# Kernel optimization log

Hardware: AMD Instinct MI355X
Metric: run time of the kernel (lower is better)

The kernel has to match this reference:

```python
import jax, jax.numpy as jnp
import numpy as np

CHEB_K = 2  # hops per support; stacked terms = 1 + 2*CHEB_K = 5


def setup_inputs() -> dict:
    key = jax.random.key(0)
    k1, k2, k3, k4, k5 = jax.random.split(key, 5)
    B, N, C, O, D = 16, 1024, 64, 64, 10
    return {
        "x": jax.random.normal(k1, (B, N, C), dtype=jnp.float32),
        "adj": jax.random.uniform(k2, (2, B, N, N), dtype=jnp.float32),
        "node_embedding": jax.random.normal(k3, (N, D), dtype=jnp.float32),
        "weights_pool": jax.random.normal(k4, (D, 2 * CHEB_K + 1, C, O), dtype=jnp.float32) * 0.1,
        "bias_pool": jax.random.normal(k5, (D, O), dtype=jnp.float32) * 0.1,
    }


def reference(x, adj, node_embedding, weights_pool, bias_pool):
    # k-hop graph aggregation over each of the 2 supports
    out = [x]
    for s in range(adj.shape[0]):
        a = adj[s]  # [B, N, N]
        x1 = x
        for _ in range(CHEB_K):
            x1 = jnp.einsum('bnm,bmc->bnc', a, x1)
            out.append(x1)
    x_g = jnp.stack(out, axis=2)  # [B, N, K, C] with K = 2*cheb_k+1 (already node-major)
    # per-node hypernetwork weights and bias from node embeddings
    weights = jnp.einsum('nd,dkio->nkio', node_embedding, weights_pool)  # [N, K, C, O]
    bias = node_embedding @ bias_pool  # [N, O]
    # per-node contraction over (K, C)
    return jnp.einsum('bnki,nkio->bno', x_g, weights) + bias
```

## Files before the change

### kernel.cpp

```cpp
#include <hip/hip_runtime.h>
#include <stdint.h>


typedef __attribute__((ext_vector_type(4))) float f32x4;
typedef __attribute__((ext_vector_type(2))) float f32x2;
typedef __attribute__((ext_vector_type(8))) short s16x8;
typedef __attribute__((ext_vector_type(8))) __bf16 bf16x8;

__device__ __forceinline__ unsigned short f2bf(float f) {
  union { float f; uint32_t u; } v; v.f = f;
  uint32_t r = v.u + 0x7FFFu + ((v.u >> 16) & 1u);
  return (unsigned short)(r >> 16);
}
__device__ __forceinline__ uint32_t pack2(float a, float b) {
  return (uint32_t)f2bf(a) | ((uint32_t)f2bf(b) << 16);
}

union FragU { s16x8 s; bf16x8 b; uint32_t u[4]; };

__device__ __forceinline__ void async_cp16(const void* g, void* l) {
  __builtin_amdgcn_global_load_lds(
      (const __attribute__((address_space(1))) void*)g,
      (__attribute__((address_space(3))) void*)l, 16, 0, 0);
}

__global__ __launch_bounds__(256) void prep(const float* __restrict__ x,
                                            const float* __restrict__ wp,
                                            unsigned short* __restrict__ XT0,
                                            unsigned short* __restrict__ wpTb) {
  __shared__ __align__(16) char smem[17160];
  const int tid = threadIdx.x;
  const int bid = blockIdx.x;
  if (bid < 256) {
    unsigned short (*tl)[72] = (unsigned short(*)[72])smem;
    const int b = bid >> 4, n0 = (bid & 15) * 64;
    {
      const int c4 = (tid & 15) * 4;
#pragma unroll
      for (int i = 0; i < 4; ++i) {
        const int row = (tid >> 4) + i * 16;
        f32x4 v =
            *(const f32x4*)(x + ((size_t)(b * 1024 + n0 + row)) * 64 + c4);
        *(uint32_t*)&tl[row][c4]     = pack2(v[0], v[1]);
        *(uint32_t*)&tl[row][c4 + 2] = pack2(v[2], v[3]);
      }
    }
    __syncthreads();
    {
      const int c = tid >> 2;
      const int nch = (tid & 3) * 16;
      s16x8 s0, s1;
#pragma unroll
      for (int j = 0; j < 8; ++j) {
        s0[j] = (short)tl[nch + j][c];
        s1[j] = (short)tl[nch + 8 + j][c];
      }
      unsigned short* p = XT0 + (size_t)(b * 64 + c) * 1024 + n0 + nch;
      *(s16x8*)p = s0;
      *(s16x8*)(p + 8) = s1;
    }
  } else {
    float (*tl)[65] = (float(*)[65])smem;
    const int jj = bid - 256;
    const int d = jj / 5, ki0 = (jj % 5) * 64;
    const float* src = wp + (size_t)d * 20480;
    {
      const int o4 = (tid & 15) * 4;
#pragma unroll
      for (int i = 0; i < 4; ++i) {
        const int row = (tid >> 4) + i * 16;
        f32x4 v = *(const f32x4*)(src + (size_t)(ki0 + row) * 64 + o4);
        tl[row][o4] = v[0]; tl[row][o4 + 1] = v[1];
        tl[row][o4 + 2] = v[2]; tl[row][o4 + 3] = v[3];
      }
    }
    __syncthreads();
    {
      const int o = tid >> 2;
      const int kch = (tid & 3) * 16;
      unsigned short* dst =
          wpTb + (size_t)d * 20480 + (size_t)o * 320 + ki0 + kch;
      s16x8 s0, s1;
#pragma unroll
      for (int j = 0; j < 8; ++j) {
        s0[j] = (short)f2bf(tl[kch + j][o]);
        s1[j] = (short)f2bf(tl[kch + 8 + j][o]);
      }
      *(s16x8*)dst = s0;
      *(s16x8*)(dst + 8) = s1;
    }
  }
}

__device__ __forceinline__ void hop_body(
    char* smem, const float* __restrict__ A,
    const unsigned short* __restrict__ XT, unsigned short* __restrict__ Xoutb,
    unsigned short* __restrict__ XTout, int write_xt, int rowbase) {
  const int tid = threadIdx.x;
  const int wave = tid >> 6, lane = tid & 63;
  const int l15 = lane & 15, q = lane >> 4;

  float* const Ast = (float*)smem;
  unsigned short* const Bst = (unsigned short*)(smem + 32768);

  const float* asrc[4];
  int aldso[4];
#pragma unroll
  for (int i = 0; i < 4; ++i) {
    const int r = wave * 16 + i * 4 + (lane >> 4);
    const int gch = (lane & 15) ^ (r & 7);
    asrc[i] = A + (size_t)(rowbase + r) * 1024 + gch * 4;
    aldso[i] = (wave * 16 + i * 4) * 64;
  }
  const unsigned short* bsrc[2];
  int bldso[2];
#pragma unroll
  for (int i = 0; i < 2; ++i) {
    const int r = wave * 16 + i * 8 + (lane >> 3);
    bsrc[i] = XT + (size_t)r * 1024 + ((lane & 7) ^ (r & 7)) * 8;
    bldso[i] = (wave * 16 + i * 8) * 64;
  }

  f32x4 acc[4];
#pragma unroll
  for (int t = 0; t < 4; ++t) acc[t] = (f32x4){0.f, 0.f, 0.f, 0.f};

  auto issue = [&](int s, int k0) {
#pragma unroll
    for (int i = 0; i < 4; ++i)
      async_cp16(asrc[i] + k0, Ast + s * 4096 + aldso[i]);
#pragma unroll
    for (int i = 0; i < 2; ++i)
      async_cp16(bsrc[i] + k0, Bst + s * 4096 + bldso[i]);
  };
  const int sw = l15 & 7;
  auto compute = [&](int s) {
    const float* Ab = Ast + s * 4096 + (wave * 16 + l15) * 64;
    const unsigned short* Bb = Bst + s * 4096 + l15 * 64;
#pragma unroll
    for (int h = 0; h < 2; ++h) {
      const int g0 = h * 8 + q * 2;
      f32x4 lo = *(const f32x4*)(Ab + (g0 ^ sw) * 4);
      f32x4 hi = *(const f32x4*)(Ab + ((g0 + 1) ^ sw) * 4);
      FragU af;
      af.u[0] = pack2(lo[0], lo[1]);
      af.u[1] = pack2(lo[2], lo[3]);
      af.u[2] = pack2(hi[0], hi[1]);
      af.u[3] = pack2(hi[2], hi[3]);
      const int cko = ((h * 4 + q) ^ sw) * 8;
#pragma unroll
      for (int t = 0; t < 4; ++t) {
        FragU bf;
        bf.s = *(const s16x8*)(Bb + t * 1024 + cko);
        acc[t] = __builtin_amdgcn_mfma_f32_16x16x32_bf16(af.b, bf.b, acc[t],
                                                         0, 0, 0);
      }
    }
  };

  issue(0, 0);
#pragma unroll 1
  for (int kt = 0; kt < 16; ++kt) {
    const int cur = kt & 1;
    __syncthreads();
    if (kt + 1 < 16) issue(cur ^ 1, (kt + 1) * 64);
    compute(cur);
  }

  __syncthreads();
  float (*tile)[65] = (float(*)[65])smem;
#pragma unroll
  for (int t = 0; t < 4; ++t)
#pragma unroll
    for (int rr = 0; rr < 4; ++rr)
      tile[wave * 16 + q * 4 + rr][t * 16 + l15] = acc[t][rr];
  __syncthreads();

  {
    const int row = tid >> 2;
    const int cb = (tid & 3) * 16;
    unsigned short* __restrict__ outp =
        Xoutb + (size_t)(rowbase + row) * 64 + cb;
    s16x8 s0, s1;
#pragma unroll
    for (int j = 0; j < 8; ++j) {
      s0[j] = (short)f2bf(tile[row][cb + j]);
      s1[j] = (short)f2bf(tile[row][cb + 8 + j]);
    }
    *(s16x8*)outp = s0;
    *(s16x8*)(outp + 8) = s1;
  }
  if (write_xt) {
    const int c = tid >> 2;
    const int nch = (tid & 3) * 16;
    unsigned short* __restrict__ xtp = XTout + (size_t)c * 1024 + rowbase + nch;
    s16x8 s0, s1;
#pragma unroll
    for (int j = 0; j < 8; ++j) {
      s0[j] = (short)f2bf(tile[nch + j][c]);
      s1[j] = (short)f2bf(tile[nch + 8 + j][c]);
    }
    *(s16x8*)xtp = s0;
    *(s16x8*)(xtp + 8) = s1;
  }
}

__global__ __launch_bounds__(256, 3) void hop1_kernel(
    const float* __restrict__ adj, const unsigned short* __restrict__ XT0,
    unsigned short* __restrict__ X1b, unsigned short* __restrict__ XT1) {
  __shared__ __align__(16) char smem[49152];
  const int bx = blockIdx.x, slice = blockIdx.y, b = slice & 15;
  hop_body(smem, adj + (size_t)slice * 1048576, XT0 + (size_t)b * 65536,
           X1b + (size_t)slice * 65536, XT1 + (size_t)slice * 65536, 1,
           bx * 64);
}

__global__ __launch_bounds__(256, 3) void hop2_kernel(
    const float* __restrict__ adj, const unsigned short* __restrict__ XT1,
    unsigned short* __restrict__ X2b) {
  __shared__ __align__(16) char smem[49152];
  const int bx = 15 - (int)blockIdx.x;
  const int slice = 31 - (int)blockIdx.y;
  hop_body(smem, adj + (size_t)slice * 1048576, XT1 + (size_t)slice * 65536,
           X2b + (size_t)slice * 65536, (unsigned short*)0, 0, bx * 64);
}

__global__ __launch_bounds__(256, 2) void final_kernel(
    const float* __restrict__ x, const unsigned short* __restrict__ X1b,
    const unsigned short* __restrict__ X2b,
    const unsigned short* __restrict__ wpTb, const float* __restrict__ emb,
    const float* __restrict__ bias_pool, float* __restrict__ out) {
  __shared__ unsigned short xg[2][16][328];
  const int tid = threadIdx.x;
  const int node_base = blockIdx.x * 2;

  for (int u = tid; u < 5120; u += 256) {
    const int nd = u / 2560;
    int rem = u - nd * 2560;
    const int bb = rem / 160;
    const int kiu = rem - bb * 160;
    const int ki = kiu * 2;
    const int k = ki >> 6;
    const int c = ki & 63;
    const int nn = node_base + nd;
    uint32_t w;
    if (k == 0) {
      f32x2 v = *(const f32x2*)(x + ((size_t)bb * 1024 + nn) * 64 + c);
      w = pack2(v[0], v[1]);
    } else {
      const unsigned short* arr = (k == 1 || k == 3) ? X1b : X2b;
      const int s = (k >= 3) ? 1 : 0;
      w = *(const uint32_t*)(arr + ((size_t)(s * 16 + bb) * 1024 + nn) * 64 + c);
    }
    *(uint32_t*)&xg[nd][bb][ki] = w;
  }
  __syncthreads();

  const int wave = tid >> 6, lane = tid & 63;
  const int nd = wave >> 1, oh = wave & 1;
  const int l15 = lane & 15, q = lane >> 4;
  const int n = node_base + nd;

  FragU af[10];
#pragma unroll
  for (int ks = 0; ks < 10; ++ks)
    af[ks].s = *(const s16x8*)&xg[nd][l15][ks * 32 + q * 8];

  f32x4 acc[2];
  acc[0] = (f32x4){0.f, 0.f, 0.f, 0.f};
  acc[1] = (f32x4){0.f, 0.f, 0.f, 0.f};

  const unsigned short* wb0 = wpTb + (size_t)(oh * 32 + l15) * 320 + q * 8;
#pragma unroll 1
  for (int d = 0; d < 10; ++d) {
    const unsigned short* wd = wb0 + (size_t)d * 20480;
    f32x4 tmp[2];
    tmp[0] = (f32x4){0.f, 0.f, 0.f, 0.f};
    tmp[1] = (f32x4){0.f, 0.f, 0.f, 0.f};
#pragma unroll
    for (int ks = 0; ks < 10; ++ks) {
#pragma unroll
      for (int tt = 0; tt < 2; ++tt) {
        FragU bf;
        bf.s = *(const s16x8*)(wd + tt * 5120 + ks * 32);
        tmp[tt] = __builtin_amdgcn_mfma_f32_16x16x32_bf16(af[ks].b, bf.b,
                                                          tmp[tt], 0, 0, 0);
      }
    }
    const float e = emb[n * 10 + d];
#pragma unroll
    for (int tt = 0; tt < 2; ++tt)
#pragma unroll
      for (int rr = 0; rr < 4; ++rr)
        acc[tt][rr] += e * tmp[tt][rr];
  }

#pragma unroll
  for (int tt = 0; tt < 2; ++tt) {
    const int o = (oh * 2 + tt) * 16 + l15;
    float bv = 0.f;
#pragma unroll
    for (int d = 0; d < 10; ++d)
      bv += emb[n * 10 + d] * bias_pool[d * 64 + o];
#pragma unroll
    for (int rr = 0; rr < 4; ++rr) {
      const int bb = q * 4 + rr;
      out[((size_t)bb * 1024 + n) * 64 + o] = acc[tt][rr] + bv;
    }
  }
}

extern "C" void kernel_launch(void* const* d_in, const int* in_sizes, int n_in,
                              void* d_out, int out_size, void* d_ws,
                              size_t ws_size, hipStream_t stream) {
  const float* x   = (const float*)d_in[0];
  const float* adj = (const float*)d_in[1];
  const float* emb = (const float*)d_in[2];
  const float* wp  = (const float*)d_in[3];
  const float* bp  = (const float*)d_in[4];
  float* out = (float*)d_out;

  char* ws = (char*)d_ws;
  unsigned short* XT0  = (unsigned short*)(ws);
  unsigned short* XT1  = (unsigned short*)(ws + ((size_t)2 << 20));
  unsigned short* X1b  = (unsigned short*)(ws + ((size_t)6 << 20));
  unsigned short* X2b  = (unsigned short*)(ws + ((size_t)10 << 20));
  unsigned short* wpTb = (unsigned short*)(ws + ((size_t)14 << 20));

  prep<<<dim3(306), dim3(256), 0, stream>>>(x, wp, XT0, wpTb);
  hop1_kernel<<<dim3(16, 32), dim3(256), 0, stream>>>(adj, XT0, X1b, XT1);
  hop2_kernel<<<dim3(16, 32), dim3(256), 0, stream>>>(adj, XT1, X2b);
  final_kernel<<<dim3(512), dim3(256), 0, stream>>>(x, X1b, X2b, wpTb, emb,
                                                    bp, out);
}
```

Baseline: 290.9 us.

## Fuse all stages into one cooperative persistent kernel with register-resident adjacency

Replaces the four launches (prep, hop1, hop2, final) with a single cooperative kernel of 256 blocks that synchronise through a software grid barrier. Each block loads its 128-row slab of the fp32 adjacency once, converts it to bf16 and keeps it in 32 register fragments, then reuses it for both hops. This halves adjacency reads from HBM, which dominate traffic. It also adds a triple-buffered pipeline for the transposed feature tiles, an X0 bf16 copy, and a swizzled weight layout staged through LDS in the final stage. In exchange it costs heavy register pressure at 512 threads, spin-barrier overhead, and a dependence on all blocks being co-resident.

```diff
diff --git a/kernel.cpp b/kernel.cpp
--- a/kernel.cpp
+++ b/kernel.cpp
@@ -3,7 +3,6 @@
 
 
 typedef __attribute__((ext_vector_type(4))) float f32x4;
-typedef __attribute__((ext_vector_type(2))) float f32x2;
 typedef __attribute__((ext_vector_type(8))) short s16x8;
 typedef __attribute__((ext_vector_type(8))) __bf16 bf16x8;
 
@@ -24,147 +23,75 @@
       (__attribute__((address_space(3))) void*)l, 16, 0, 0);
 }
 
-__global__ __launch_bounds__(256) void prep(const float* __restrict__ x,
-                                            const float* __restrict__ wp,
-                                            unsigned short* __restrict__ XT0,
-                                            unsigned short* __restrict__ wpTb) {
-  __shared__ __align__(16) char smem[17160];
-  const int tid = threadIdx.x;
-  const int bid = blockIdx.x;
-  if (bid < 256) {
-    unsigned short (*tl)[72] = (unsigned short(*)[72])smem;
-    const int b = bid >> 4, n0 = (bid & 15) * 64;
-    {
-      const int c4 = (tid & 15) * 4;
-#pragma unroll
-      for (int i = 0; i < 4; ++i) {
-        const int row = (tid >> 4) + i * 16;
-        f32x4 v =
-            *(const f32x4*)(x + ((size_t)(b * 1024 + n0 + row)) * 64 + c4);
-        *(uint32_t*)&tl[row][c4]     = pack2(v[0], v[1]);
-        *(uint32_t*)&tl[row][c4 + 2] = pack2(v[2], v[3]);
-      }
-    }
-    __syncthreads();
-    {
-      const int c = tid >> 2;
-      const int nch = (tid & 3) * 16;
-      s16x8 s0, s1;
-#pragma unroll
-      for (int j = 0; j < 8; ++j) {
-        s0[j] = (short)tl[nch + j][c];
-        s1[j] = (short)tl[nch + 8 + j][c];
-      }
-      unsigned short* p = XT0 + (size_t)(b * 64 + c) * 1024 + n0 + nch;
-      *(s16x8*)p = s0;
-      *(s16x8*)(p + 8) = s1;
-    }
-  } else {
-    float (*tl)[65] = (float(*)[65])smem;
-    const int jj = bid - 256;
-    const int d = jj / 5, ki0 = (jj % 5) * 64;
-    const float* src = wp + (size_t)d * 20480;
-    {
-      const int o4 = (tid & 15) * 4;
-#pragma unroll
-      for (int i = 0; i < 4; ++i) {
-        const int row = (tid >> 4) + i * 16;
-        f32x4 v = *(const f32x4*)(src + (size_t)(ki0 + row) * 64 + o4);
-        tl[row][o4] = v[0]; tl[row][o4 + 1] = v[1];
-        tl[row][o4 + 2] = v[2]; tl[row][o4 + 3] = v[3];
-      }
-    }
-    __syncthreads();
-    {
-      const int o = tid >> 2;
-      const int kch = (tid & 3) * 16;
-      unsigned short* dst =
-          wpTb + (size_t)d * 20480 + (size_t)o * 320 + ki0 + kch;
-      s16x8 s0, s1;
-#pragma unroll
-      for (int j = 0; j < 8; ++j) {
-        s0[j] = (short)f2bf(tl[kch + j][o]);
-        s1[j] = (short)f2bf(tl[kch + 8 + j][o]);
-      }
-      *(s16x8*)dst = s0;
-      *(s16x8*)(dst + 8) = s1;
-    }
-  }
-}
-
-__device__ __forceinline__ void hop_body(
-    char* smem, const float* __restrict__ A,
-    const unsigned short* __restrict__ XT, unsigned short* __restrict__ Xoutb,
-    unsigned short* __restrict__ XTout, int write_xt, int rowbase) {
+__global__ __launch_bounds__(64) void init_bar(unsigned* bar) {
+  if (threadIdx.x < 2) bar[threadIdx.x] = 0u;
+}
+
+__device__ __forceinline__ void gbar(unsigned* bar) {
+  __syncthreads();
+  if (threadIdx.x == 0) {
+    __threadfence();
+    unsigned g = __hip_atomic_load(bar + 1, __ATOMIC_RELAXED,
+                                   __HIP_MEMORY_SCOPE_AGENT);
+    unsigned a = __hip_atomic_fetch_add(bar, 1u, __ATOMIC_ACQ_REL,
+                                        __HIP_MEMORY_SCOPE_AGENT);
+    if (a == 255u) {
+      __hip_atomic_store(bar, 0u, __ATOMIC_RELAXED, __HIP_MEMORY_SCOPE_AGENT);
+      __hip_atomic_store(bar + 1, g + 1u, __ATOMIC_RELEASE,
+                         __HIP_MEMORY_SCOPE_AGENT);
+    } else {
+      while (__hip_atomic_load(bar + 1, __ATOMIC_RELAXED,
+                               __HIP_MEMORY_SCOPE_AGENT) == g)
+        __builtin_amdgcn_s_sleep(2);
+    }
+    __threadfence();
+  }
+  __syncthreads();
+}
+
+__device__ __forceinline__ void hop128(char* smem, const FragU (&af)[32],
+                                       const unsigned short* __restrict__ XT,
+                                       unsigned short* __restrict__ Xoutb,
+                                       unsigned short* __restrict__ XTout,
+                                       const int write_xt) {
   const int tid = threadIdx.x;
   const int wave = tid >> 6, lane = tid & 63;
-  const int l15 = lane & 15, q = lane >> 4;
-
-  float* const Ast = (float*)smem;
-  unsigned short* const Bst = (unsigned short*)(smem + 32768);
-
-  const float* asrc[4];
-  int aldso[4];
-#pragma unroll
-  for (int i = 0; i < 4; ++i) {
-    const int r = wave * 16 + i * 4 + (lane >> 4);
-    const int gch = (lane & 15) ^ (r & 7);
-    asrc[i] = A + (size_t)(rowbase + r) * 1024 + gch * 4;
-    aldso[i] = (wave * 16 + i * 4) * 64;
-  }
-  const unsigned short* bsrc[2];
-  int bldso[2];
-#pragma unroll
-  for (int i = 0; i < 2; ++i) {
-    const int r = wave * 16 + i * 8 + (lane >> 3);
-    bsrc[i] = XT + (size_t)r * 1024 + ((lane & 7) ^ (r & 7)) * 8;
-    bldso[i] = (wave * 16 + i * 8) * 64;
-  }
+  const int l15 = lane & 15, q = lane >> 4, sw = l15 & 7;
+
+  unsigned short* const Bst = (unsigned short*)smem;
+  const int c = wave * 8 + (lane >> 3);
+  const unsigned short* bsrc =
+      XT + (size_t)c * 1024 + ((lane & 7) ^ (c & 7)) * 8;
+  unsigned short* const bdst = Bst + wave * 512;
 
   f32x4 acc[4];
 #pragma unroll
   for (int t = 0; t < 4; ++t) acc[t] = (f32x4){0.f, 0.f, 0.f, 0.f};
 
-  auto issue = [&](int s, int k0) {
-#pragma unroll
-    for (int i = 0; i < 4; ++i)
-      async_cp16(asrc[i] + k0, Ast + s * 4096 + aldso[i]);
-#pragma unroll
-    for (int i = 0; i < 2; ++i)
-      async_cp16(bsrc[i] + k0, Bst + s * 4096 + bldso[i]);
-  };
-  const int sw = l15 & 7;
-  auto compute = [&](int s) {
-    const float* Ab = Ast + s * 4096 + (wave * 16 + l15) * 64;
-    const unsigned short* Bb = Bst + s * 4096 + l15 * 64;
-#pragma unroll
-    for (int h = 0; h < 2; ++h) {
-      const int g0 = h * 8 + q * 2;
-      f32x4 lo = *(const f32x4*)(Ab + (g0 ^ sw) * 4);
-      f32x4 hi = *(const f32x4*)(Ab + ((g0 + 1) ^ sw) * 4);
-      FragU af;
-      af.u[0] = pack2(lo[0], lo[1]);
-      af.u[1] = pack2(lo[2], lo[3]);
-      af.u[2] = pack2(hi[0], hi[1]);
-      af.u[3] = pack2(hi[2], hi[3]);
-      const int cko = ((h * 4 + q) ^ sw) * 8;
+  asm volatile("s_waitcnt vmcnt(0)" ::: "memory");
+  async_cp16(bsrc, bdst);
+  async_cp16(bsrc + 64, bdst + 4096);
+#pragma unroll
+  for (int kt = 0; kt < 16; ++kt) {
+    if (kt == 15) asm volatile("s_waitcnt vmcnt(0)" ::: "memory");
+    else          asm volatile("s_waitcnt vmcnt(1)" ::: "memory");
+    __builtin_amdgcn_sched_barrier(0);
+    __builtin_amdgcn_s_barrier();
+    __builtin_amdgcn_sched_barrier(0);
+    if (kt + 2 < 16)
+      async_cp16(bsrc + (kt + 2) * 64, bdst + ((kt + 2) % 3) * 4096);
+    const unsigned short* Bb = Bst + (kt % 3) * 4096 + l15 * 64;
+#pragma unroll
+    for (int kk = 0; kk < 2; ++kk) {
+      const int p = ((kk * 4 + q) ^ sw) * 8;
 #pragma unroll
       for (int t = 0; t < 4; ++t) {
         FragU bf;
-        bf.s = *(const s16x8*)(Bb + t * 1024 + cko);
-        acc[t] = __builtin_amdgcn_mfma_f32_16x16x32_bf16(af.b, bf.b, acc[t],
-                                                         0, 0, 0);
-      }
-    }
-  };
-
-  issue(0, 0);
-#pragma unroll 1
-  for (int kt = 0; kt < 16; ++kt) {
-    const int cur = kt & 1;
-    __syncthreads();
-    if (kt + 1 < 16) issue(cur ^ 1, (kt + 1) * 64);
-    compute(cur);
+        bf.s = *(const s16x8*)(Bb + t * 1024 + p);
+        acc[t] = __builtin_amdgcn_mfma_f32_16x16x32_bf16(
+            af[kt * 2 + kk].b, bf.b, acc[t], 0, 0, 0);
+      }
+    }
   }
 
   __syncthreads();
@@ -175,137 +102,200 @@
     for (int rr = 0; rr < 4; ++rr)
       tile[wave * 16 + q * 4 + rr][t * 16 + l15] = acc[t][rr];
   __syncthreads();
-
   {
-    const int row = tid >> 2;
-    const int cb = (tid & 3) * 16;
-    unsigned short* __restrict__ outp =
-        Xoutb + (size_t)(rowbase + row) * 64 + cb;
+    const int row = tid >> 2, cb = (tid & 3) * 16;
     s16x8 s0, s1;
 #pragma unroll
     for (int j = 0; j < 8; ++j) {
       s0[j] = (short)f2bf(tile[row][cb + j]);
       s1[j] = (short)f2bf(tile[row][cb + 8 + j]);
     }
+    unsigned short* outp = Xoutb + (size_t)row * 64 + cb;
     *(s16x8*)outp = s0;
     *(s16x8*)(outp + 8) = s1;
   }
   if (write_xt) {
-    const int c = tid >> 2;
-    const int nch = (tid & 3) * 16;
-    unsigned short* __restrict__ xtp = XTout + (size_t)c * 1024 + rowbase + nch;
+    const int c2 = tid >> 3, nch = (tid & 7) * 16;
     s16x8 s0, s1;
 #pragma unroll
     for (int j = 0; j < 8; ++j) {
-      s0[j] = (short)f2bf(tile[nch + j][c]);
-      s1[j] = (short)f2bf(tile[nch + 8 + j][c]);
-    }
+      s0[j] = (short)f2bf(tile[nch + j][c2]);
+      s1[j] = (short)f2bf(tile[nch + 8 + j][c2]);
+    }
+    unsigned short* xtp = XTout + (size_t)c2 * 1024 + nch;
     *(s16x8*)xtp = s0;
     *(s16x8*)(xtp + 8) = s1;
   }
 }
 
-__global__ __launch_bounds__(256, 3) void hop1_kernel(
-    const float* __restrict__ adj, const unsigned short* __restrict__ XT0,
-    unsigned short* __restrict__ X1b, unsigned short* __restrict__ XT1) {
+__global__ __launch_bounds__(512, 2) void mega(
+    const float* __restrict__ adj, const float* __restrict__ x,
+    const float* __restrict__ emb, const float* __restrict__ wp,
+    const float* __restrict__ bp, float* __restrict__ out,
+    unsigned short* __restrict__ XT0, unsigned short* __restrict__ X0b,
+    unsigned short* __restrict__ XT1, unsigned short* __restrict__ X1b,
+    unsigned short* __restrict__ X2b, unsigned short* __restrict__ wpTb,
+    unsigned* bar) {
   __shared__ __align__(16) char smem[49152];
-  const int bx = blockIdx.x, slice = blockIdx.y, b = slice & 15;
-  hop_body(smem, adj + (size_t)slice * 1048576, XT0 + (size_t)b * 65536,
-           X1b + (size_t)slice * 65536, XT1 + (size_t)slice * 65536, 1,
-           bx * 64);
-}
-
-__global__ __launch_bounds__(256, 3) void hop2_kernel(
-    const float* __restrict__ adj, const unsigned short* __restrict__ XT1,
-    unsigned short* __restrict__ X2b) {
-  __shared__ __align__(16) char smem[49152];
-  const int bx = 15 - (int)blockIdx.x;
-  const int slice = 31 - (int)blockIdx.y;
-  hop_body(smem, adj + (size_t)slice * 1048576, XT1 + (size_t)slice * 65536,
-           X2b + (size_t)slice * 65536, (unsigned short*)0, 0, bx * 64);
-}
-
-__global__ __launch_bounds__(256, 2) void final_kernel(
-    const float* __restrict__ x, const unsigned short* __restrict__ X1b,
-    const unsigned short* __restrict__ X2b,
-    const unsigned short* __restrict__ wpTb, const float* __restrict__ emb,
-    const float* __restrict__ bias_pool, float* __restrict__ out) {
-  __shared__ unsigned short xg[2][16][328];
-  const int tid = threadIdx.x;
-  const int node_base = blockIdx.x * 2;
-
-  for (int u = tid; u < 5120; u += 256) {
-    const int nd = u / 2560;
-    int rem = u - nd * 2560;
-    const int bb = rem / 160;
-    const int kiu = rem - bb * 160;
-    const int ki = kiu * 2;
-    const int k = ki >> 6;
-    const int c = ki & 63;
-    const int nn = node_base + nd;
-    uint32_t w;
-    if (k == 0) {
-      f32x2 v = *(const f32x2*)(x + ((size_t)bb * 1024 + nn) * 64 + c);
-      w = pack2(v[0], v[1]);
-    } else {
-      const unsigned short* arr = (k == 1 || k == 3) ? X1b : X2b;
-      const int s = (k >= 3) ? 1 : 0;
-      w = *(const uint32_t*)(arr + ((size_t)(s * 16 + bb) * 1024 + nn) * 64 + c);
-    }
-    *(uint32_t*)&xg[nd][bb][ki] = w;
-  }
-  __syncthreads();
-
+  const int tid = threadIdx.x, bid = blockIdx.x;
   const int wave = tid >> 6, lane = tid & 63;
-  const int nd = wave >> 1, oh = wave & 1;
   const int l15 = lane & 15, q = lane >> 4;
-  const int n = node_base + nd;
-
-  FragU af[10];
-#pragma unroll
-  for (int ks = 0; ks < 10; ++ks)
-    af[ks].s = *(const s16x8*)&xg[nd][l15][ks * 32 + q * 8];
-
-  f32x4 acc[2];
-  acc[0] = (f32x4){0.f, 0.f, 0.f, 0.f};
-  acc[1] = (f32x4){0.f, 0.f, 0.f, 0.f};
-
-  const unsigned short* wb0 = wpTb + (size_t)(oh * 32 + l15) * 320 + q * 8;
+
+  if (tid < 256) {
+    unsigned short (*tl)[72] = (unsigned short(*)[72])smem;
+    const int b = bid >> 4, n0 = (bid & 15) * 64;
+    const int c4 = (tid & 15) * 4;
+#pragma unroll
+    for (int i = 0; i < 4; ++i) {
+      const int row = (tid >> 4) + i * 16;
+      f32x4 v = *(const f32x4*)(x + ((size_t)(b * 1024 + n0 + row)) * 64 + c4);
+      const uint32_t w0 = pack2(v[0], v[1]);
+      const uint32_t w1 = pack2(v[2], v[3]);
+      *(uint32_t*)&tl[row][c4] = w0;
+      *(uint32_t*)&tl[row][c4 + 2] = w1;
+      const uint64_t wq = (uint64_t)w0 | ((uint64_t)w1 << 32);
+      *(uint64_t*)(X0b + ((size_t)(b * 1024 + n0 + row)) * 64 + c4) = wq;
+    }
+  } else if (bid < 50) {
+    float (*tlw)[65] = (float(*)[65])(smem + 18432);
+    const int t2 = tid - 256;
+    const int d = bid / 5, ki0 = (bid % 5) * 64;
+    const float* src = wp + (size_t)d * 20480;
+    const int o4 = (t2 & 15) * 4;
+#pragma unroll
+    for (int i = 0; i < 4; ++i) {
+      const int row = (t2 >> 4) + i * 16;
+      f32x4 v = *(const f32x4*)(src + (size_t)(ki0 + row) * 64 + o4);
+      tlw[row][o4] = v[0]; tlw[row][o4 + 1] = v[1];
+      tlw[row][o4 + 2] = v[2]; tlw[row][o4 + 3] = v[3];
+    }
+  }
+  __syncthreads();
+  if (tid < 256) {
+    unsigned short (*tl)[72] = (unsigned short(*)[72])smem;
+    const int b = bid >> 4, n0 = (bid & 15) * 64;
+    const int cc = tid >> 2, nch = (tid & 3) * 16;
+    s16x8 s0, s1;
+#pragma unroll
+    for (int j = 0; j < 8; ++j) {
+      s0[j] = (short)tl[nch + j][cc];
+      s1[j] = (short)tl[nch + 8 + j][cc];
+    }
+    unsigned short* p = XT0 + (size_t)(b * 64 + cc) * 1024 + n0 + nch;
+    *(s16x8*)p = s0;
+    *(s16x8*)(p + 8) = s1;
+  } else if (bid < 50) {
+    float (*tlw)[65] = (float(*)[65])(smem + 18432);
+    const int t2 = tid - 256;
+    const int d = bid / 5, ki0 = (bid % 5) * 64;
+    const int o = t2 >> 2, kch = (t2 & 3) * 16;
+    s16x8 s0, s1;
+#pragma unroll
+    for (int j = 0; j < 8; ++j) {
+      s0[j] = (short)f2bf(tlw[kch + j][o]);
+      s1[j] = (short)f2bf(tlw[kch + 8 + j][o]);
+    }
+    const int c0 = (ki0 + kch) >> 3;
+    unsigned short* base = wpTb + (size_t)d * 24576 + (size_t)o * 384;
+    *(s16x8*)(base + ((c0) ^ (o & 7)) * 8) = s0;
+    *(s16x8*)(base + ((c0 + 1) ^ (o & 7)) * 8) = s1;
+  }
+
+  const int slice = bid >> 3;
+  const int rowbase = (bid & 7) * 128;
+  const float* arow =
+      adj + ((size_t)slice * 1024 + rowbase + wave * 16 + l15) * 1024 + q * 8;
+  FragU af[32];
+#pragma unroll
+  for (int ks = 0; ks < 32; ++ks) {
+    f32x4 lo = *(const f32x4*)(arow + ks * 32);
+    f32x4 hi = *(const f32x4*)(arow + ks * 32 + 4);
+    af[ks].u[0] = pack2(lo[0], lo[1]);
+    af[ks].u[1] = pack2(lo[2], lo[3]);
+    af[ks].u[2] = pack2(hi[0], hi[1]);
+    af[ks].u[3] = pack2(hi[2], hi[3]);
+  }
+
+  gbar(bar);
+
+  hop128(smem, af, XT0 + (size_t)(slice & 15) * 65536,
+         X1b + (size_t)slice * 65536 + (size_t)rowbase * 64,
+         XT1 + (size_t)slice * 65536 + rowbase, 1);
+
+  gbar(bar);
+
+  hop128(smem, af, XT1 + (size_t)slice * 65536,
+         X2b + (size_t)slice * 65536 + (size_t)rowbase * 64,
+         (unsigned short*)0, 0);
+
+  gbar(bar);
+
+  {
+    unsigned short (*wd)[384] = (unsigned short(*)[384])smem;
+    const int nd = wave >> 1, oh = wave & 1;
+    const int n = bid * 4 + nd;
+    const int sw2 = l15 & 7;
+
+    FragU af10[10];
+#pragma unroll
+    for (int ks = 0; ks < 10; ++ks) {
+      const int k = ks >> 1;
+      const int cc0 = (ks & 1) * 32 + q * 8;
+      const unsigned short* srcp;
+      if (k == 0) {
+        srcp = X0b + ((size_t)l15 * 1024 + n) * 64 + cc0;
+      } else {
+        const unsigned short* arr = (k == 1 || k == 3) ? X1b : X2b;
+        const int s = (k >= 3) ? 1 : 0;
+        srcp = arr + ((size_t)(s * 16 + l15) * 1024 + n) * 64 + cc0;
+      }
+      af10[ks].s = *(const s16x8*)srcp;
+    }
+
+    f32x4 acc0 = {0.f, 0.f, 0.f, 0.f}, acc1 = {0.f, 0.f, 0.f, 0.f};
+    const unsigned short* wsrc = wpTb + (size_t)wave * 3072 + lane * 8;
+    unsigned short* wdst = (unsigned short*)smem + wave * 3072;
 #pragma unroll 1
-  for (int d = 0; d < 10; ++d) {
-    const unsigned short* wd = wb0 + (size_t)d * 20480;
-    f32x4 tmp[2];
-    tmp[0] = (f32x4){0.f, 0.f, 0.f, 0.f};
-    tmp[1] = (f32x4){0.f, 0.f, 0.f, 0.f};
-#pragma unroll
-    for (int ks = 0; ks < 10; ++ks) {
-#pragma unroll
-      for (int tt = 0; tt < 2; ++tt) {
-        FragU bf;
-        bf.s = *(const s16x8*)(wd + tt * 5120 + ks * 32);
-        tmp[tt] = __builtin_amdgcn_mfma_f32_16x16x32_bf16(af[ks].b, bf.b,
-                                                          tmp[tt], 0, 0, 0);
-      }
-    }
-    const float e = emb[n * 10 + d];
-#pragma unroll
-    for (int tt = 0; tt < 2; ++tt)
-#pragma unroll
-      for (int rr = 0; rr < 4; ++rr)
-        acc[tt][rr] += e * tmp[tt][rr];
-  }
-
-#pragma unroll
-  for (int tt = 0; tt < 2; ++tt) {
-    const int o = (oh * 2 + tt) * 16 + l15;
-    float bv = 0.f;
-#pragma unroll
-    for (int d = 0; d < 10; ++d)
-      bv += emb[n * 10 + d] * bias_pool[d * 64 + o];
-#pragma unroll
-    for (int rr = 0; rr < 4; ++rr) {
-      const int bb = q * 4 + rr;
-      out[((size_t)bb * 1024 + n) * 64 + o] = acc[tt][rr] + bv;
+    for (int d = 0; d < 10; ++d) {
+      if (d) __syncthreads();
+#pragma unroll
+      for (int i = 0; i < 6; ++i)
+        async_cp16(wsrc + (size_t)d * 24576 + i * 512, wdst + i * 512);
+      asm volatile("s_waitcnt vmcnt(0)" ::: "memory");
+      __builtin_amdgcn_sched_barrier(0);
+      __syncthreads();
+      f32x4 t0 = {0.f, 0.f, 0.f, 0.f}, t1 = {0.f, 0.f, 0.f, 0.f};
+#pragma unroll
+      for (int ks = 0; ks < 10; ++ks) {
+        const int p = ((ks * 4 + q) ^ sw2) * 8;
+        FragU b0, b1;
+        b0.s = *(const s16x8*)&wd[oh * 32 + l15][p];
+        b1.s = *(const s16x8*)&wd[oh * 32 + 16 + l15][p];
+        t0 = __builtin_amdgcn_mfma_f32_16x16x32_bf16(af10[ks].b, b0.b, t0,
+                                                     0, 0, 0);
+        t1 = __builtin_amdgcn_mfma_f32_16x16x32_bf16(af10[ks].b, b1.b, t1,
+                                                     0, 0, 0);
+      }
+      const float e = emb[n * 10 + d];
+#pragma unroll
+      for (int rr = 0; rr < 4; ++rr) {
+        acc0[rr] += e * t0[rr];
+        acc1[rr] += e * t1[rr];
+      }
+    }
+
+#pragma unroll
+    for (int tt = 0; tt < 2; ++tt) {
+      const int o = oh * 32 + tt * 16 + l15;
+      float bv = 0.f;
+#pragma unroll
+      for (int d = 0; d < 10; ++d) bv += emb[n * 10 + d] * bp[d * 64 + o];
+#pragma unroll
+      for (int rr = 0; rr < 4; ++rr) {
+        const int bb = q * 4 + rr;
+        const float a = tt ? acc1[rr] : acc0[rr];
+        out[((size_t)bb * 1024 + n) * 64 + o] = a + bv;
+      }
     }
   }
 }
@@ -322,14 +312,19 @@
 
   char* ws = (char*)d_ws;
   unsigned short* XT0  = (unsigned short*)(ws);
-  unsigned short* XT1  = (unsigned short*)(ws + ((size_t)2 << 20));
-  unsigned short* X1b  = (unsigned short*)(ws + ((size_t)6 << 20));
-  unsigned short* X2b  = (unsigned short*)(ws + ((size_t)10 << 20));
-  unsigned short* wpTb = (unsigned short*)(ws + ((size_t)14 << 20));
-
-  prep<<<dim3(306), dim3(256), 0, stream>>>(x, wp, XT0, wpTb);
-  hop1_kernel<<<dim3(16, 32), dim3(256), 0, stream>>>(adj, XT0, X1b, XT1);
-  hop2_kernel<<<dim3(16, 32), dim3(256), 0, stream>>>(adj, XT1, X2b);
-  final_kernel<<<dim3(512), dim3(256), 0, stream>>>(x, X1b, X2b, wpTb, emb,
-                                                    bp, out);
-}
+  unsigned short* X0b  = (unsigned short*)(ws + ((size_t)2 << 20));
+  unsigned short* XT1  = (unsigned short*)(ws + ((size_t)4 << 20));
+  unsigned short* X1b  = (unsigned short*)(ws + ((size_t)8 << 20));
+  unsigned short* X2b  = (unsigned short*)(ws + ((size_t)12 << 20));
+  unsigned short* wpTb = (unsigned short*)(ws + ((size_t)16 << 20));
+  unsigned* bar        = (unsigned*)(ws + ((size_t)17 << 20));
+
+  init_bar<<<dim3(1), dim3(64), 0, stream>>>(bar);
+
+  void* args[] = {(void*)&adj, (void*)&x,   (void*)&emb, (void*)&wp,
+                  (void*)&bp,  (void*)&out, (void*)&XT0, (void*)&X0b,
+                  (void*)&XT1, (void*)&X1b, (void*)&X2b, (void*)&wpTb,
+                  (void*)&bar};
+  hipLaunchCooperativeKernel((void*)mega, dim3(256), dim3(512), args, 0,
+                             stream);
+}
```

Result: slower. 385.9 us (+32.7%).
